# Performance work log

Hardware: AMD Instinct MI355X
Metric: run time of the kernel (lower is better)

Reference implementation:

```python
import jax, jax.numpy as jnp
import numpy as np

BS, GRID, LSTM_H, CNN_C, PROJ = 256, 49, 512, 2048, 512


def setup_inputs() -> dict:
    key = jax.random.key(0)
    ks = jax.random.split(key, 7)
    s = lambda fan_in: 1.0 / np.sqrt(fan_in)
    return {
        "lstm_hidden": jax.random.normal(ks[0], (BS, LSTM_H), jnp.float32),
        "cnn_feat": jax.random.normal(ks[1], (BS, GRID, CNN_C), jnp.float32),
        "W_lstm": jax.random.normal(ks[2], (PROJ, LSTM_H), jnp.float32) * s(LSTM_H),
        "b_lstm": jax.random.normal(ks[3], (PROJ,), jnp.float32) * s(LSTM_H),
        "W_cnn": jax.random.normal(ks[4], (PROJ, CNN_C), jnp.float32) * s(CNN_C),
        "b_cnn": jax.random.normal(ks[5], (PROJ,), jnp.float32) * s(CNN_C),
        "w_attn": jax.random.normal(ks[6], (1, PROJ), jnp.float32) * s(PROJ),
    }


def reference(lstm_hidden, cnn_feat, W_lstm, b_lstm, W_cnn, b_cnn, w_attn):
    # H computed once (original loop recomputes it per grid, identically)
    H = lstm_hidden @ W_lstm.T + b_lstm                       # (bs, P)
    V = jnp.einsum("bgc,pc->bgp", cnn_feat, W_cnn) + b_cnn    # (bs, G, P)
    z = jnp.tanh(H[:, None, :] + V) @ w_attn[0]               # (bs, G)
    bs, G = z.shape
    # Faithful to torch: cat over grids along dim 0 -> (G*bs,), then view(bs, G)
    z_scrambled = jnp.swapaxes(z, 0, 1).reshape(bs, G)
    return jax.nn.softmax(z_scrambled, axis=1)
```

## Files before the change

### kernel.cpp

```cpp
#include <hip/hip_runtime.h>
#include <math.h>

#define BSZ    256
#define GRID_N 49
#define LSTMH  512
#define CNN_C  2048
#define PROJ   512
#define KAUG   2560
#define M_TOT  12544
#define BK     64
#define KTILES (KAUG / BK)

#define MT2    128
#define NT2    128
#define NBLK2  ((M_TOT / MT2) * (PROJ / NT2))

#define MT     64
#define NT     128
#define NBLK   ((M_TOT / MT) * (PROJ / NT))

#define ACHUNKS (M_TOT * CNN_C / 8)
#define LCHUNKS (BSZ * LSTMH / 8)
#define ABLK    ((ACHUNKS + LCHUNKS) / 256)
#define WBLK    640
#define PBLK    (ABLK + WBLK)

typedef short bf16x8 __attribute__((ext_vector_type(8)));
typedef float f32x4  __attribute__((ext_vector_type(4)));

static __device__ __forceinline__ unsigned short bf16_rne(float f) {
    unsigned int u = __float_as_uint(f);
    u = u + 0x7FFFu + ((u >> 16) & 1u);
    return (unsigned short)(u >> 16);
}
static __device__ __forceinline__ uint4 pack8f(const float* f) {
    uint4 o;
    o.x = (unsigned int)bf16_rne(f[0]) | ((unsigned int)bf16_rne(f[1]) << 16);
    o.y = (unsigned int)bf16_rne(f[2]) | ((unsigned int)bf16_rne(f[3]) << 16);
    o.z = (unsigned int)bf16_rne(f[4]) | ((unsigned int)bf16_rne(f[5]) << 16);
    o.w = (unsigned int)bf16_rne(f[6]) | ((unsigned int)bf16_rne(f[7]) << 16);
    return o;
}
static __device__ __forceinline__ float tanh_fast(float x) {
    float e = __expf(2.f * x);
    return 1.f - 2.f / (e + 1.f);
}
static __device__ __forceinline__ void glds16(const void* g, void* l) {
    __builtin_amdgcn_global_load_lds(
        (const __attribute__((address_space(1))) unsigned int*)g,
        (__attribute__((address_space(3))) unsigned int*)l, 16, 0, 0);
}

__global__ __launch_bounds__(256) void prep_all(
    const float* __restrict__ cnn, const float* __restrict__ lstm,
    const float* __restrict__ Wc,  const float* __restrict__ Wl,
    unsigned short* __restrict__ wsW, unsigned short* __restrict__ wsA,
    unsigned short* __restrict__ wsL, float* __restrict__ out)
{
    const int bid = blockIdx.x, t = threadIdx.x;
    if (bid < 49) out[bid * 256 + t] = 0.f;
    float f[8];
    if (bid < ABLK) {
        const int c = bid * 256 + t;
        const float* src; unsigned short* dst;
        if (c < ACHUNKS) { src = cnn  + (size_t)c * 8; dst = wsA + (size_t)c * 8; }
        else { const int c2 = c - ACHUNKS; src = lstm + (size_t)c2 * 8; dst = wsL + (size_t)c2 * 8; }
        *(float4*)&f[0] = ((const float4*)src)[0];
        *(float4*)&f[4] = ((const float4*)src)[1];
        *(uint4*)dst = pack8f(f);
    } else {
        const int c  = (bid - ABLK) * 256 + t;
        const int p  = c / 320;
        const int kc = (c % 320) * 8;
        const float* src = (kc < CNN_C) ? (Wc + (size_t)p * CNN_C + kc)
                                        : (Wl + (size_t)p * LSTMH + (kc - CNN_C));
        *(float4*)&f[0] = ((const float4*)src)[0];
        *(float4*)&f[4] = ((const float4*)src)[1];
        *(uint4*)(wsW + (size_t)p * KAUG + kc) = pack8f(f);
    }
}

__global__ __launch_bounds__(512, 4) void gemm4(
    const unsigned short* __restrict__ wsW, const unsigned short* __restrict__ wsA,
    const unsigned short* __restrict__ wsL,
    const float* __restrict__ bl, const float* __restrict__ bc,
    const float* __restrict__ wat, float* __restrict__ out)
{
    __shared__ unsigned short Ab[2][MT2][BK];
    __shared__ unsigned short Bb[2][NT2][BK];

    const int t   = threadIdx.x;
    const int w   = t >> 6;
    const int l   = t & 63;
    const int q   = l >> 4;
    const int r16 = l & 15;
    const int wr  = w >> 2;
    const int wc  = w & 3;

    const int bid = (int)blockIdx.x;
    const int swz = (bid & 7) * (NBLK2 / 8) + (bid >> 3);
    const int m0  = (swz >> 2) * MT2;
    const int n0  = (swz & 3) * NT2;

    const int srow = l >> 3;
    const int cg   = (l & 7) ^ srow;

    auto stage = [&](int kt, int bufi) {
        const int k0 = kt * BK;
        #pragma unroll
        for (int j = 0; j < 2; ++j) {
            const int rowb = w * 16 + j * 8;
            const unsigned short* g = wsW + (size_t)(n0 + rowb + srow) * KAUG + k0 + cg * 8;
            glds16(g, &Bb[bufi][rowb][0]);
        }
        if (k0 < CNN_C) {
            #pragma unroll
            for (int j = 0; j < 2; ++j) {
                const int rowa = w * 16 + j * 8;
                const unsigned short* g = wsA + (size_t)(m0 + rowa + srow) * CNN_C + k0 + cg * 8;
                glds16(g, &Ab[bufi][rowa][0]);
            }
        } else {
            const int k0l = k0 - CNN_C;
            #pragma unroll
            for (int j = 0; j < 2; ++j) {
                const int rowa = w * 16 + j * 8;
                const int rg   = m0 + rowa + srow;
                const unsigned short* g = wsL + (size_t)(rg / 49) * LSTMH + k0l + cg * 8;
                glds16(g, &Ab[bufi][rowa][0]);
            }
        }
    };

    f32x4 acc[4][2];
    #pragma unroll
    for (int mt = 0; mt < 4; ++mt)
        #pragma unroll
        for (int nt = 0; nt < 2; ++nt)
            acc[mt][nt] = (f32x4){0.f, 0.f, 0.f, 0.f};

    stage(0, 0);
    asm volatile("s_waitcnt vmcnt(0)" ::: "memory");
    __builtin_amdgcn_s_barrier();

    int cur = 0;
    for (int kt = 0; kt < KTILES; ++kt) {
        if (kt + 1 < KTILES) stage(kt + 1, cur ^ 1);
        __builtin_amdgcn_s_setprio(1);
        #pragma unroll
        for (int ks = 0; ks < 2; ++ks) {
            const int cp = ((ks * 4 + q) ^ (r16 & 7)) * 8;
            bf16x8 af[4], bfr[2];
            #pragma unroll
            for (int mt = 0; mt < 4; ++mt)
                af[mt] = *(const bf16x8*)&Ab[cur][wr * 64 + mt * 16 + r16][cp];
            #pragma unroll
            for (int nt = 0; nt < 2; ++nt)
                bfr[nt] = *(const bf16x8*)&Bb[cur][wc * 32 + nt * 16 + r16][cp];
            #pragma unroll
            for (int mt = 0; mt < 4; ++mt)
                #pragma unroll
                for (int nt = 0; nt < 2; ++nt)
                    acc[mt][nt] = __builtin_amdgcn_mfma_f32_16x16x32_bf16(
                        af[mt], bfr[nt], acc[mt][nt], 0, 0, 0);
        }
        __builtin_amdgcn_s_setprio(0);
        asm volatile("s_waitcnt vmcnt(0) lgkmcnt(0)" ::: "memory");
        __builtin_amdgcn_s_barrier();
        cur ^= 1;
    }

    float* zpf = (float*)&Ab[0][0][0];
    float part[4][4];
    #pragma unroll
    for (int mt = 0; mt < 4; ++mt)
        #pragma unroll
        for (int rr = 0; rr < 4; ++rr) part[mt][rr] = 0.f;
    #pragma unroll
    for (int nt = 0; nt < 2; ++nt) {
        const int p = n0 + wc * 32 + nt * 16 + r16;
        const float bb = bl[p] + bc[p];
        const float wa = wat[p];
        #pragma unroll
        for (int mt = 0; mt < 4; ++mt)
            #pragma unroll
            for (int rr = 0; rr < 4; ++rr)
                part[mt][rr] += tanh_fast(acc[mt][nt][rr] + bb) * wa;
    }
    #pragma unroll
    for (int mt = 0; mt < 4; ++mt)
        #pragma unroll
        for (int rr = 0; rr < 4; ++rr) {
            float v = part[mt][rr];
            v += __shfl_xor(v, 1);
            v += __shfl_xor(v, 2);
            v += __shfl_xor(v, 4);
            v += __shfl_xor(v, 8);
            if (r16 == 0) zpf[wc * MT2 + wr * 64 + mt * 16 + q * 4 + rr] = v;
        }
    __syncthreads();
    if (t < MT2) {
        const float v = zpf[t] + zpf[MT2 + t] + zpf[2 * MT2 + t] + zpf[3 * MT2 + t];
        const int row = m0 + t;
        const int b2  = row / 49;
        const int g2  = row - b2 * 49;
        atomicAdd(&out[g2 * BSZ + b2], v);
    }
}

__global__ __launch_bounds__(256, 4) void gemm_k(
    const float* __restrict__ lstm, const float* __restrict__ cnn,
    const float* __restrict__ Wc,   const float* __restrict__ Wl,
    const float* __restrict__ bl,   const float* __restrict__ bc,
    const float* __restrict__ wat,  float* __restrict__ out)
{
    __shared__ unsigned short Ash[MT][BK];
    __shared__ unsigned short Bsh[NT][BK];
    __shared__ float zp[4][MT];

    const int t   = threadIdx.x;
    const int w   = t >> 6;
    const int l   = t & 63;
    const int q   = l >> 4;
    const int r16 = l & 15;

    const int bid = (int)blockIdx.x;
    const int swz = (bid & 7) * (NBLK / 8) + (bid >> 3);
    const int m0 = (swz >> 2) * MT;
    const int n0 = (swz & 3) * NT;

    const int ra  = t >> 2;
    const int ca0 = t & 3;
    const int sa  = ra & 7;
    const int grow = m0 + ra;
    const int ab   = grow / 49;
    const int ag   = grow - ab * 49;
    const float* cnnb  = cnn + ((size_t)ab * GRID_N + ag) * CNN_C;
    const float* lstmb = lstm + (size_t)ab * LSTMH;

    f32x4 acc[4][2];
    #pragma unroll
    for (int mt = 0; mt < 4; ++mt)
        #pragma unroll
        for (int nt = 0; nt < 2; ++nt)
            acc[mt][nt] = (f32x4){0.f, 0.f, 0.f, 0.f};

    float4 fa0, fa1, fa2, fa3;

    auto a_load = [&](int k0) {
        const float* s = (k0 < CNN_C) ? (cnnb + k0) : (lstmb + (k0 - CNN_C));
        const float4* p0 = (const float4*)(s + ca0 * 8);
        const float4* p1 = (const float4*)(s + (ca0 + 4) * 8);
        fa0 = p0[0]; fa1 = p0[1];
        fa2 = p1[0]; fa3 = p1[1];
    };
    auto a_write = [&]() {
        float f[8];
        *(float4*)&f[0] = fa0; *(float4*)&f[4] = fa1;
        *(uint4*)&Ash[ra][(ca0 ^ sa) * 8] = pack8f(f);
        *(float4*)&f[0] = fa2; *(float4*)&f[4] = fa3;
        *(uint4*)&Ash[ra][((ca0 + 4) ^ sa) * 8] = pack8f(f);
    };
    auto b_stage = [&](int k0) {
        const int rb = t >> 1;
        const int hb = t & 1;
        const float* s = (k0 < CNN_C) ? (Wc + (size_t)(n0 + rb) * CNN_C + k0)
                                      : (Wl + (size_t)(n0 + rb) * LSTMH + (k0 - CNN_C));
        const int sw = rb & 7;
        #pragma unroll
        for (int c = 0; c < 4; ++c) {
            const int cc = hb * 4 + c;
            float f[8];
            *(float4*)&f[0] = ((const float4*)(s + cc * 8))[0];
            *(float4*)&f[4] = ((const float4*)(s + cc * 8))[1];
            *(uint4*)&Bsh[rb][(cc ^ sw) * 8] = pack8f(f);
        }
    };

    a_load(0);
    a_write();
    b_stage(0);

    for (int kt = 0; kt < KTILES; ++kt) {
        __syncthreads();
        const bool more = (kt + 1 < KTILES);
        if (more) a_load((kt + 1) * BK);
        #pragma unroll
        for (int ks = 0; ks < 2; ++ks) {
            const int cp = ((ks * 4 + q) ^ (r16 & 7)) * 8;
            bf16x8 af[4], bfr[2];
            #pragma unroll
            for (int mt = 0; mt < 4; ++mt)
                af[mt] = *(const bf16x8*)&Ash[mt * 16 + r16][cp];
            #pragma unroll
            for (int nt = 0; nt < 2; ++nt)
                bfr[nt] = *(const bf16x8*)&Bsh[w * 32 + nt * 16 + r16][cp];
            #pragma unroll
            for (int mt = 0; mt < 4; ++mt)
                #pragma unroll
                for (int nt = 0; nt < 2; ++nt)
                    acc[mt][nt] = __builtin_amdgcn_mfma_f32_16x16x32_bf16(
                        af[mt], bfr[nt], acc[mt][nt], 0, 0, 0);
        }
        __syncthreads();
        if (more) { a_write(); b_stage((kt + 1) * BK); }
    }

    float part[4][4];
    #pragma unroll
    for (int mt = 0; mt < 4; ++mt)
        #pragma unroll
        for (int rr = 0; rr < 4; ++rr) part[mt][rr] = 0.f;
    #pragma unroll
    for (int nt = 0; nt < 2; ++nt) {
        const int p = n0 + w * 32 + nt * 16 + r16;
        const float bb = bl[p] + bc[p];
        const float wa = wat[p];
        #pragma unroll
        for (int mt = 0; mt < 4; ++mt)
            #pragma unroll
            for (int rr = 0; rr < 4; ++rr)
                part[mt][rr] += tanh_fast(acc[mt][nt][rr] + bb) * wa;
    }
    #pragma unroll
    for (int mt = 0; mt < 4; ++mt)
        #pragma unroll
        for (int rr = 0; rr < 4; ++rr) {
            float v = part[mt][rr];
            v += __shfl_xor(v, 1);
            v += __shfl_xor(v, 2);
            v += __shfl_xor(v, 4);
            v += __shfl_xor(v, 8);
            if (r16 == 0) zp[w][mt * 16 + q * 4 + rr] = v;
        }
    __syncthreads();
    if (t < MT) {
        const float v = zp[0][t] + zp[1][t] + zp[2][t] + zp[3][t];
        const int row = m0 + t;
        const int b2  = row / 49;
        const int g2  = row - b2 * 49;
        atomicAdd(&out[g2 * BSZ + b2], v);
    }
}

__global__ __launch_bounds__(64) void softmax_rows(float* __restrict__ out)
{
    const int i = blockIdx.x;
    const int j = threadIdx.x;
    float x = (j < GRID_N) ? out[i * GRID_N + j] : -1e30f;
    float m = x;
    #pragma unroll
    for (int off = 32; off > 0; off >>= 1) m = fmaxf(m, __shfl_xor(m, off));
    float e = (j < GRID_N) ? __expf(x - m) : 0.f;
    float s = e;
    #pragma unroll
    for (int off = 32; off > 0; off >>= 1) s += __shfl_xor(s, off);
    if (j < GRID_N) out[i * GRID_N + j] = e / s;
}

extern "C" void kernel_launch(void* const* d_in, const int* in_sizes, int n_in,
                              void* d_out, int out_size, void* d_ws, size_t ws_size,
                              hipStream_t stream)
{
    const float* lstm = (const float*)d_in[0];
    const float* cnn  = (const float*)d_in[1];
    const float* Wl   = (const float*)d_in[2];
    const float* bl   = (const float*)d_in[3];
    const float* Wc   = (const float*)d_in[4];
    const float* bc   = (const float*)d_in[5];
    const float* wat  = (const float*)d_in[6];
    float* out = (float*)d_out;

    const size_t szW = (size_t)PROJ * KAUG * sizeof(unsigned short);
    const size_t szA = (size_t)M_TOT * CNN_C * sizeof(unsigned short);
    const size_t szL = (size_t)BSZ * LSTMH * sizeof(unsigned short);

    if (ws_size >= szW + szA + szL) {
        unsigned short* wsW = (unsigned short*)d_ws;
        unsigned short* wsA = wsW + (size_t)PROJ * KAUG;
        unsigned short* wsL = wsA + (size_t)M_TOT * CNN_C;
        prep_all<<<dim3(PBLK), dim3(256), 0, stream>>>(cnn, lstm, Wc, Wl, wsW, wsA, wsL, out);
        gemm4<<<dim3(NBLK2), dim3(512), 0, stream>>>(wsW, wsA, wsL, bl, bc, wat, out);
    } else {
        hipMemsetAsync(out, 0, (size_t)out_size * sizeof(float), stream);
        gemm_k<<<dim3(NBLK), dim3(256), 0, stream>>>(lstm, cnn, Wc, Wl, bl, bc, wat, out);
    }
    softmax_rows<<<dim3(BSZ), dim3(64), 0, stream>>>(out);
}
```

Measured before the change: 217.6 us.

## Use 4-wave 128x128 GEMM tiles with single-buffered LDS and 64x64 warp tiles

Replaces the 8-wave double-buffered 128x128 GEMM with a 4-wave version. Each wave now computes a 64x64 sub-tile (4x4 MFMA accumulators) instead of 64x32, which raises register-level reuse of the A and B fragments. LDS is single-buffered, with the next tile loaded after a barrier once compute finishes, so there is no longer any overlap between global loads and MFMA inside a block. The design relies on having more resident blocks per CU to hide load latency, and accepts the larger accumulator register footprint and the lost intra-block prefetch.

```diff
diff --git a/kernel.cpp b/kernel.cpp
--- a/kernel.cpp
+++ b/kernel.cpp
@@ -80,22 +80,22 @@
     }
 }
 
-__global__ __launch_bounds__(512, 4) void gemm4(
+__global__ __launch_bounds__(256, 4) void gemm5(
     const unsigned short* __restrict__ wsW, const unsigned short* __restrict__ wsA,
     const unsigned short* __restrict__ wsL,
     const float* __restrict__ bl, const float* __restrict__ bc,
     const float* __restrict__ wat, float* __restrict__ out)
 {
-    __shared__ unsigned short Ab[2][MT2][BK];
-    __shared__ unsigned short Bb[2][NT2][BK];
+    __shared__ unsigned short Ash[MT2][BK];
+    __shared__ unsigned short Bsh[NT2][BK];
 
     const int t   = threadIdx.x;
     const int w   = t >> 6;
     const int l   = t & 63;
     const int q   = l >> 4;
     const int r16 = l & 15;
-    const int wr  = w >> 2;
-    const int wc  = w & 3;
+    const int wr  = w >> 1;
+    const int wc  = w & 1;
 
     const int bid = (int)blockIdx.x;
     const int swz = (bid & 7) * (NBLK2 / 8) + (bid >> 3);
@@ -105,80 +105,75 @@
     const int srow = l >> 3;
     const int cg   = (l & 7) ^ srow;
 
-    auto stage = [&](int kt, int bufi) {
+    auto stage = [&](int kt) {
         const int k0 = kt * BK;
         #pragma unroll
-        for (int j = 0; j < 2; ++j) {
-            const int rowb = w * 16 + j * 8;
+        for (int j = 0; j < 4; ++j) {
+            const int rowb = w * 32 + j * 8;
             const unsigned short* g = wsW + (size_t)(n0 + rowb + srow) * KAUG + k0 + cg * 8;
-            glds16(g, &Bb[bufi][rowb][0]);
+            glds16(g, &Bsh[rowb][0]);
         }
         if (k0 < CNN_C) {
             #pragma unroll
-            for (int j = 0; j < 2; ++j) {
-                const int rowa = w * 16 + j * 8;
+            for (int j = 0; j < 4; ++j) {
+                const int rowa = w * 32 + j * 8;
                 const unsigned short* g = wsA + (size_t)(m0 + rowa + srow) * CNN_C + k0 + cg * 8;
-                glds16(g, &Ab[bufi][rowa][0]);
+                glds16(g, &Ash[rowa][0]);
             }
         } else {
             const int k0l = k0 - CNN_C;
             #pragma unroll
-            for (int j = 0; j < 2; ++j) {
-                const int rowa = w * 16 + j * 8;
+            for (int j = 0; j < 4; ++j) {
+                const int rowa = w * 32 + j * 8;
                 const int rg   = m0 + rowa + srow;
                 const unsigned short* g = wsL + (size_t)(rg / 49) * LSTMH + k0l + cg * 8;
-                glds16(g, &Ab[bufi][rowa][0]);
+                glds16(g, &Ash[rowa][0]);
             }
         }
     };
 
-    f32x4 acc[4][2];
-    #pragma unroll
-    for (int mt = 0; mt < 4; ++mt)
-        #pragma unroll
-        for (int nt = 0; nt < 2; ++nt)
+    f32x4 acc[4][4];
+    #pragma unroll
+    for (int mt = 0; mt < 4; ++mt)
+        #pragma unroll
+        for (int nt = 0; nt < 4; ++nt)
             acc[mt][nt] = (f32x4){0.f, 0.f, 0.f, 0.f};
 
-    stage(0, 0);
-    asm volatile("s_waitcnt vmcnt(0)" ::: "memory");
-    __builtin_amdgcn_s_barrier();
-
-    int cur = 0;
+    stage(0);
+
     for (int kt = 0; kt < KTILES; ++kt) {
-        if (kt + 1 < KTILES) stage(kt + 1, cur ^ 1);
-        __builtin_amdgcn_s_setprio(1);
+        asm volatile("s_waitcnt vmcnt(0)" ::: "memory");
+        __builtin_amdgcn_s_barrier();
         #pragma unroll
         for (int ks = 0; ks < 2; ++ks) {
             const int cp = ((ks * 4 + q) ^ (r16 & 7)) * 8;
-            bf16x8 af[4], bfr[2];
+            bf16x8 af[4], bfr[4];
             #pragma unroll
             for (int mt = 0; mt < 4; ++mt)
-                af[mt] = *(const bf16x8*)&Ab[cur][wr * 64 + mt * 16 + r16][cp];
-            #pragma unroll
-            for (int nt = 0; nt < 2; ++nt)
-                bfr[nt] = *(const bf16x8*)&Bb[cur][wc * 32 + nt * 16 + r16][cp];
+                af[mt] = *(const bf16x8*)&Ash[wr * 64 + mt * 16 + r16][cp];
+            #pragma unroll
+            for (int nt = 0; nt < 4; ++nt)
+                bfr[nt] = *(const bf16x8*)&Bsh[wc * 64 + nt * 16 + r16][cp];
             #pragma unroll
             for (int mt = 0; mt < 4; ++mt)
                 #pragma unroll
-                for (int nt = 0; nt < 2; ++nt)
+                for (int nt = 0; nt < 4; ++nt)
                     acc[mt][nt] = __builtin_amdgcn_mfma_f32_16x16x32_bf16(
                         af[mt], bfr[nt], acc[mt][nt], 0, 0, 0);
         }
-        __builtin_amdgcn_s_setprio(0);
-        asm volatile("s_waitcnt vmcnt(0) lgkmcnt(0)" ::: "memory");
         __builtin_amdgcn_s_barrier();
-        cur ^= 1;
-    }
-
-    float* zpf = (float*)&Ab[0][0][0];
+        if (kt + 1 < KTILES) stage(kt + 1);
+    }
+
+    float* zpf = (float*)&Ash[0][0];
     float part[4][4];
     #pragma unroll
     for (int mt = 0; mt < 4; ++mt)
         #pragma unroll
         for (int rr = 0; rr < 4; ++rr) part[mt][rr] = 0.f;
     #pragma unroll
-    for (int nt = 0; nt < 2; ++nt) {
-        const int p = n0 + wc * 32 + nt * 16 + r16;
+    for (int nt = 0; nt < 4; ++nt) {
+        const int p = n0 + wc * 64 + nt * 16 + r16;
         const float bb = bl[p] + bc[p];
         const float wa = wat[p];
         #pragma unroll
@@ -200,7 +195,7 @@
         }
     __syncthreads();
     if (t < MT2) {
-        const float v = zpf[t] + zpf[MT2 + t] + zpf[2 * MT2 + t] + zpf[3 * MT2 + t];
+        const float v = zpf[t] + zpf[MT2 + t];
         const int row = m0 + t;
         const int b2  = row / 49;
         const int g2  = row - b2 * 49;
@@ -380,7 +375,7 @@
         unsigned short* wsA = wsW + (size_t)PROJ * KAUG;
         unsigned short* wsL = wsA + (size_t)M_TOT * CNN_C;
         prep_all<<<dim3(PBLK), dim3(256), 0, stream>>>(cnn, lstm, Wc, Wl, wsW, wsA, wsL, out);
-        gemm4<<<dim3(NBLK2), dim3(512), 0, stream>>>(wsW, wsA, wsL, bl, bc, wat, out);
+        gemm5<<<dim3(NBLK2), dim3(256), 0, stream>>>(wsW, wsA, wsL, bl, bc, wat, out);
     } else {
         hipMemsetAsync(out, 0, (size_t)out_size * sizeof(float), stream);
         gemm_k<<<dim3(NBLK), dim3(256), 0, stream>>>(lstm, cnn, Wc, Wl, bl, bc, wat, out);
```

After: 217.8 us. No clear change (+0.1%).
